# Kernel tuning notes

Hardware: AMD Instinct MI355X
Metric: run time of the kernel (lower is better)

The kernel has to match this reference:

```python
import jax, jax.numpy as jnp
import numpy as np

B, C, T, H, W = 8, 1024, 8, 28, 28
E = C // 2  # embed_dim = 512
EPS = 1e-5


def conv1x1(x, w, b):
    # x: [B,C,T,H,W], w: [O,C], b: [O] -> [B,O,T,H,W]
    return jnp.einsum('bcthw,oc->bothw', x, w) + b[None, :, None, None, None]


def maxpool_122(x):
    # MaxPool3d(kernel=(1,2,2)), stride = kernel, VALID padding
    return jax.lax.reduce_window(
        x, -jnp.inf, jax.lax.max,
        window_dimensions=(1, 1, 1, 2, 2),
        window_strides=(1, 1, 1, 2, 2),
        padding='VALID')


def setup_inputs() -> dict:
    key = jax.random.key(0)
    ks = jax.random.split(key, 10)
    s_in = 1.0 / np.sqrt(C)
    s_e = 1.0 / np.sqrt(E)
    return {
        'x': jax.random.normal(ks[0], (B, C, T, H, W), dtype=jnp.float32),
        'w_theta': jax.random.normal(ks[1], (E, C), dtype=jnp.float32) * s_in,
        'b_theta': jnp.zeros((E,), dtype=jnp.float32),
        'w_phi': jax.random.normal(ks[2], (E, C), dtype=jnp.float32) * s_in,
        'b_phi': jnp.zeros((E,), dtype=jnp.float32),
        'w_g': jax.random.normal(ks[3], (E, C), dtype=jnp.float32) * s_in,
        'b_g': jnp.zeros((E,), dtype=jnp.float32),
        'w_out': jax.random.normal(ks[4], (C, E), dtype=jnp.float32) * s_e,
        'b_out': jnp.zeros((C,), dtype=jnp.float32),
        'bn_gamma': jnp.ones((C,), dtype=jnp.float32),
        'bn_beta': jnp.zeros((C,), dtype=jnp.float32),
        'bn_mean': jnp.zeros((C,), dtype=jnp.float32),
        'bn_var': jnp.ones((C,), dtype=jnp.float32),
    }


def reference(x, w_theta, b_theta, w_phi, b_phi, w_g, b_g,
              w_out, b_out, bn_gamma, bn_beta, bn_mean, bn_var):
    # embed projections (phi/g applied after (1,2,2) max-pool sub-sampling)
    theta = conv1x1(x, w_theta, b_theta).reshape(B, E, -1)      # [B,E,N]
    x_sub = maxpool_122(x)                                       # [B,C,T,H/2,W/2]
    phi = conv1x1(x_sub, w_phi, b_phi).reshape(B, E, -1)         # [B,E,M]
    g = conv1x1(x_sub, w_g, b_g).reshape(B, E, -1)               # [B,E,M]

    # gaussian non-local: softmax(theta^T phi) over keys
    scores = jnp.einsum('ben,bem->bnm', theta, phi)              # [B,N,M]
    p = jax.nn.softmax(scores, axis=2)

    y = jnp.einsum('bem,bnm->ben', g, p).reshape(B, E, T, H, W)  # [B,E,T,H,W]

    # W conv + BN (inference stats) + residual
    z = conv1x1(y, w_out, b_out)
    inv = jax.lax.rsqrt(bn_var + EPS)
    z = (z - bn_mean[None, :, None, None, None]) * (bn_gamma * inv)[None, :, None, None, None] \
        + bn_beta[None, :, None, None, None]
    return z + x
```

## Files before the change

kernel.cpp:

```cpp
#include <hip/hip_runtime.h>
#include <cstddef>

typedef _Float16 f16x8 __attribute__((ext_vector_type(8)));
typedef float f32x4 __attribute__((ext_vector_type(4)));

#define B_ 8
#define C_ 1024
#define T_ 8
#define H_ 28
#define W_ 28
#define E_ 512
#define N_ (T_*H_*W_)
#define M_ (T_*(H_/2)*(W_/2))

__device__ __forceinline__ void gld16(const _Float16* g, _Float16* l) {
    __builtin_amdgcn_global_load_lds((const __attribute__((address_space(1))) void*)g,
                                     (__attribute__((address_space(3))) void*)l, 16, 0, 0);
}

__global__ void prep_kernel(const float* __restrict__ wt, const float* __restrict__ wp,
                            const float* __restrict__ wg, const float* __restrict__ wo,
                            const float* __restrict__ b_out,
                            const float* __restrict__ gamma, const float* __restrict__ beta,
                            const float* __restrict__ mean, const float* __restrict__ var,
                            _Float16* __restrict__ wt_h, _Float16* __restrict__ wp_h,
                            _Float16* __restrict__ wg_h, _Float16* __restrict__ wo_h,
                            float* __restrict__ scale, float* __restrict__ shift,
                            int nW, int nC)
{
    int i = blockIdx.x * blockDim.x + threadIdx.x;
    if (i < nW) {
        wt_h[i] = (_Float16)wt[i];
        wp_h[i] = (_Float16)wp[i];
        wg_h[i] = (_Float16)wg[i];
        wo_h[i] = (_Float16)wo[i];
    }
    if (i < nC) {
        float sc = gamma[i] * rsqrtf(var[i] + 1e-5f);
        scale[i] = sc;
        shift[i] = (b_out[i] - mean[i]) * sc + beta[i];
    }
}

__global__ void xt_kernel(const float* __restrict__ x, _Float16* __restrict__ XT)
{
    __shared__ float sm[32][33];
    int n0 = blockIdx.x * 32, c0 = blockIdx.y * 32, b = blockIdx.z;
    const float* xb = x + (size_t)b * C_ * N_;
    _Float16* xtb = XT + (size_t)b * N_ * C_;
#pragma unroll
    for (int i = 0; i < 4; i++) {
        int c = c0 + threadIdx.y + i * 8;
        sm[threadIdx.y + i * 8][threadIdx.x] = xb[(size_t)c * N_ + n0 + threadIdx.x];
    }
    __syncthreads();
#pragma unroll
    for (int i = 0; i < 4; i++) {
        int n = n0 + threadIdx.y + i * 8;
        xtb[(size_t)n * C_ + c0 + threadIdx.x] = (_Float16)sm[threadIdx.x][threadIdx.y + i * 8];
    }
}

__global__ void pool_kernel(const float* __restrict__ x, _Float16* __restrict__ XST)
{
    __shared__ float sm[32][33];
    const int H2 = H_ / 2, W2 = W_ / 2, HW = H_ * W_;
    int m0 = blockIdx.x * 32, c0 = blockIdx.y * 32, b = blockIdx.z;
    const float* xb = x + (size_t)b * C_ * T_ * HW;
#pragma unroll
    for (int i = 0; i < 4; i++) {
        int c = c0 + threadIdx.y + i * 8;
        int m = m0 + threadIdx.x;
        int t = m / (H2 * W2);
        int r = m - t * (H2 * W2);
        int h2 = r / W2;
        int w2 = r - h2 * W2;
        const float* p = xb + ((size_t)c * T_ + t) * HW + (h2 * 2) * W_ + w2 * 2;
        float v0 = fmaxf(p[0], p[1]);
        float v1 = fmaxf(p[W_], p[W_ + 1]);
        sm[threadIdx.y + i * 8][threadIdx.x] = fmaxf(v0, v1);
    }
    __syncthreads();
#pragma unroll
    for (int i = 0; i < 4; i++) {
        int m = m0 + threadIdx.y + i * 8;
        XST[((size_t)b * M_ + m) * C_ + c0 + threadIdx.x] = (_Float16)sm[threadIdx.x][threadIdx.y + i * 8];
    }
}

__global__ void softmax_kernel(_Float16* __restrict__ S, int rows)
{
    int wave = threadIdx.x >> 6, lane = threadIdx.x & 63;
    int row = blockIdx.x * 4 + wave;
    if (row >= rows) return;
    _Float16* s = S + (size_t)row * M_;
    f16x8 v[4];
    bool val[4];
    float mx = -3.4e38f;
#pragma unroll
    for (int it = 0; it < 4; it++) {
        int base = it * 512 + lane * 8;
        val[it] = (base < M_);
        if (val[it]) {
            v[it] = *(const f16x8*)(s + base);
#pragma unroll
            for (int q = 0; q < 8; q++) mx = fmaxf(mx, (float)v[it][q]);
        }
    }
#pragma unroll
    for (int off = 32; off > 0; off >>= 1) mx = fmaxf(mx, __shfl_xor(mx, off, 64));
    float ev[32];
    float sum = 0.f;
#pragma unroll
    for (int it = 0; it < 4; it++) {
        if (val[it]) {
#pragma unroll
            for (int q = 0; q < 8; q++) {
                float e = __expf((float)v[it][q] - mx);
                ev[it * 8 + q] = e;
                sum += e;
            }
        }
    }
#pragma unroll
    for (int off = 32; off > 0; off >>= 1) sum += __shfl_xor(sum, off, 64);
    float inv = 1.f / sum;
#pragma unroll
    for (int it = 0; it < 4; it++) {
        if (val[it]) {
            f16x8 o;
#pragma unroll
            for (int q = 0; q < 8; q++) o[q] = (_Float16)(ev[it * 8 + q] * inv);
            *(f16x8*)(s + it * 512 + lane * 8) = o;
        }
    }
}

template<int BIAS, int EPI>
__global__ __launch_bounds__(256, 2)
void gemm_nt(const _Float16* __restrict__ A, const _Float16* __restrict__ B,
             void* __restrict__ Cout, const float* __restrict__ bias,
             const float* __restrict__ scale, const float* __restrict__ shift,
             const float* __restrict__ resid,
             int Mdim, int Ndim, int K,
             long long strideA, long long strideB, long long strideC)
{
    __shared__ alignas(16) _Float16 As[128 * 32];
    __shared__ alignas(16) _Float16 Bs[128 * 32];
    __shared__ alignas(16) float eps_[32 * 132];

    const int tid = threadIdx.x;
    const int lane = tid & 63;
    const int wave = tid >> 6;
    const int wm = wave >> 1, wn = wave & 1;
    const int lane15 = lane & 15, quad = lane >> 4;

    const int m0 = blockIdx.y * 128;
    const int n0 = blockIdx.x * 128;
    const int bz = blockIdx.z;
    A += (size_t)bz * strideA;
    B += (size_t)bz * strideB;

    const int c0 = wave * 128 + lane;
    const int c1 = c0 + 64;
    const int ar0 = min(m0 + (c0 >> 2), Mdim - 1);
    const int ar1 = min(m0 + (c1 >> 2), Mdim - 1);
    const int br0 = min(n0 + (c0 >> 2), Ndim - 1);
    const int br1 = min(n0 + (c1 >> 2), Ndim - 1);
    const _Float16* ap0 = A + (size_t)ar0 * K + (c0 & 3) * 8;
    const _Float16* ap1 = A + (size_t)ar1 * K + (c1 & 3) * 8;
    const _Float16* bp0 = B + (size_t)br0 * K + (c0 & 3) * 8;
    const _Float16* bp1 = B + (size_t)br1 * K + (c1 & 3) * 8;
    _Float16* lA0 = As + wave * 1024;
    _Float16* lA1 = As + wave * 1024 + 512;
    _Float16* lB0 = Bs + wave * 1024;
    _Float16* lB1 = Bs + wave * 1024 + 512;

    f32x4 acc[4][4];
#pragma unroll
    for (int i = 0; i < 4; i++)
#pragma unroll
        for (int j = 0; j < 4; j++)
            acc[i][j] = (f32x4){0.f, 0.f, 0.f, 0.f};

    for (int k0 = 0; k0 < K; k0 += 32) {
        __syncthreads();
        gld16(ap0 + k0, lA0);
        gld16(ap1 + k0, lA1);
        gld16(bp0 + k0, lB0);
        gld16(bp1 + k0, lB1);
        __syncthreads();

        f16x8 af[4], bf[4];
#pragma unroll
        for (int i = 0; i < 4; i++)
            af[i] = *(const f16x8*)&As[(wm * 64 + i * 16 + lane15) * 32 + quad * 8];
#pragma unroll
        for (int j = 0; j < 4; j++)
            bf[j] = *(const f16x8*)&Bs[(wn * 64 + j * 16 + lane15) * 32 + quad * 8];
#pragma unroll
        for (int i = 0; i < 4; i++)
#pragma unroll
            for (int j = 0; j < 4; j++)
                acc[i][j] = __builtin_amdgcn_mfma_f32_16x16x32_f16(af[i], bf[j], acc[i][j], 0, 0, 0);
    }

    const size_t cbase = (size_t)bz * strideC;
#pragma unroll
    for (int i = 0; i < 4; i++) {
        __syncthreads();
#pragma unroll
        for (int j = 0; j < 4; j++) {
            int col = wn * 64 + j * 16 + lane15;
#pragma unroll
            for (int r = 0; r < 4; r++)
                eps_[(wm * 16 + quad * 4 + r) * 132 + col] = acc[i][j][r];
        }
        __syncthreads();
        if (EPI == 2) {
            int rg = tid >> 5, cc = tid & 31;
#pragma unroll
            for (int r = 0; r < 4; r++) {
                int lr = rg * 4 + r;
                int grow = m0 + (lr >> 4) * 64 + i * 16 + (lr & 15);
                int gcol = n0 + cc * 4;
                size_t idx = cbase + (size_t)grow * Ndim + gcol;
                f32x4 v = *(const f32x4*)&eps_[lr * 132 + cc * 4];
                f32x4 res = *(const f32x4*)&resid[idx];
                float sc = scale[grow], sh = shift[grow];
                f32x4 o;
#pragma unroll
                for (int q = 0; q < 4; q++) o[q] = v[q] * sc + sh + res[q];
                *(f32x4*)&((float*)Cout)[idx] = o;
            }
        } else {
            int rg = tid >> 4, cc8 = tid & 15;
#pragma unroll
            for (int r2 = 0; r2 < 2; r2++) {
                int lr = rg * 2 + r2;
                int grow = m0 + (lr >> 4) * 64 + i * 16 + (lr & 15);
                int gcol = n0 + cc8 * 8;
                if (grow < Mdim && gcol < Ndim) {
                    f16x8 o;
#pragma unroll
                    for (int q = 0; q < 8; q++) {
                        float v2 = eps_[lr * 132 + cc8 * 8 + q];
                        if (BIAS == 1) v2 += bias[gcol + q];
                        if (BIAS == 2) v2 += bias[grow];
                        o[q] = (_Float16)v2;
                    }
                    *(f16x8*)&((_Float16*)Cout)[cbase + (size_t)grow * Ndim + gcol] = o;
                }
            }
        }
    }
}

extern "C" void kernel_launch(void* const* d_in, const int* in_sizes, int n_in,
                              void* d_out, int out_size, void* d_ws, size_t ws_size,
                              hipStream_t stream)
{
    const float* x       = (const float*)d_in[0];
    const float* w_theta = (const float*)d_in[1];
    const float* b_theta = (const float*)d_in[2];
    const float* w_phi   = (const float*)d_in[3];
    const float* b_phi   = (const float*)d_in[4];
    const float* w_g     = (const float*)d_in[5];
    const float* b_g     = (const float*)d_in[6];
    const float* w_out   = (const float*)d_in[7];
    const float* b_out   = (const float*)d_in[8];
    const float* gamma   = (const float*)d_in[9];
    const float* beta    = (const float*)d_in[10];
    const float* mean    = (const float*)d_in[11];
    const float* var     = (const float*)d_in[12];
    float* out = (float*)d_out;
    (void)in_sizes; (void)n_in; (void)out_size;

    char* ws = (char*)d_ws;
    size_t off = 0;
    auto alloc = [&](size_t bytes) -> void* {
        off = (off + 255) & ~(size_t)255;
        void* p = ws + off;
        off += bytes;
        return p;
    };

    _Float16* wt_h = (_Float16*)alloc((size_t)E_ * C_ * 2);
    _Float16* wp_h = (_Float16*)alloc((size_t)E_ * C_ * 2);
    _Float16* wg_h = (_Float16*)alloc((size_t)E_ * C_ * 2);
    _Float16* wo_h = (_Float16*)alloc((size_t)C_ * E_ * 2);
    float* scale   = (float*)alloc((size_t)C_ * 4);
    float* shift   = (float*)alloc((size_t)C_ * 4);
    _Float16* XT   = (_Float16*)alloc((size_t)B_ * N_ * C_ * 2);
    _Float16* XST  = (_Float16*)alloc((size_t)B_ * M_ * C_ * 2);
    _Float16* Th   = (_Float16*)alloc((size_t)B_ * N_ * E_ * 2);
    _Float16* Ph   = (_Float16*)alloc((size_t)B_ * M_ * E_ * 2);
    _Float16* Gb   = (_Float16*)alloc((size_t)B_ * E_ * M_ * 2);
    _Float16* Yt   = (_Float16*)alloc((size_t)B_ * N_ * E_ * 2);

    size_t sz_s_all = (size_t)B_ * N_ * M_ * 2;
    bool batched = ws_size > off + sz_s_all + 65536;
    _Float16* Sall = (_Float16*)alloc(batched ? sz_s_all : (size_t)N_ * M_ * 2);

    prep_kernel<<<dim3((E_ * C_) / 256), dim3(256), 0, stream>>>(
        w_theta, w_phi, w_g, w_out, b_out, gamma, beta, mean, var,
        wt_h, wp_h, wg_h, wo_h, scale, shift, E_ * C_, C_);

    xt_kernel<<<dim3(N_ / 32, C_ / 32, B_), dim3(32, 8), 0, stream>>>(x, XT);
    pool_kernel<<<dim3(M_ / 32, C_ / 32, B_), dim3(32, 8), 0, stream>>>(x, XST);

    gemm_nt<1, 0><<<dim3(E_ / 128, N_ / 128, B_), dim3(256), 0, stream>>>(
        XT, wt_h, Th, b_theta, nullptr, nullptr, nullptr,
        N_, E_, C_, (long long)N_ * C_, 0, (long long)N_ * E_);

    gemm_nt<1, 0><<<dim3(E_ / 128, (M_ + 127) / 128, B_), dim3(256), 0, stream>>>(
        XST, wp_h, Ph, b_phi, nullptr, nullptr, nullptr,
        M_, E_, C_, (long long)M_ * C_, 0, (long long)M_ * E_);

    gemm_nt<2, 0><<<dim3((M_ + 127) / 128, E_ / 128, B_), dim3(256), 0, stream>>>(
        wg_h, XST, Gb, b_g, nullptr, nullptr, nullptr,
        E_, M_, C_, 0, (long long)M_ * C_, (long long)E_ * M_);

    const int nbz = batched ? B_ : 1;
    for (int b0 = 0; b0 < B_; b0 += nbz) {
        gemm_nt<0, 0><<<dim3((M_ + 127) / 128, N_ / 128, nbz), dim3(256), 0, stream>>>(
            Th + (size_t)b0 * N_ * E_, Ph + (size_t)b0 * M_ * E_, Sall,
            nullptr, nullptr, nullptr, nullptr,
            N_, M_, E_, (long long)N_ * E_, (long long)M_ * E_, (long long)N_ * M_);

        softmax_kernel<<<dim3((nbz * N_) / 4), dim3(256), 0, stream>>>(Sall, nbz * N_);

        gemm_nt<0, 0><<<dim3(E_ / 128, N_ / 128, nbz), dim3(256), 0, stream>>>(
            Sall, Gb + (size_t)b0 * E_ * M_, Yt + (size_t)b0 * N_ * E_,
            nullptr, nullptr, nullptr, nullptr,
            N_, E_, M_, (long long)N_ * M_, (long long)E_ * M_, (long long)N_ * E_);
    }

    gemm_nt<0, 2><<<dim3(N_ / 128, C_ / 128, B_), dim3(256), 0, stream>>>(
        wo_h, Yt, out, nullptr, scale, shift, x,
        C_, N_, E_, 0, (long long)N_ * E_, (long long)C_ * N_);
}
```

Measured before the change: 998.5 us.

## Add 256x256 8-wave pipelined MFMA GEMM and pad key dimension to 1792

Adds a new gemm8 kernel that uses 256x256 tiles with 512 threads, double-buffered LDS filled by direct global-to-LDS loads, XOR-swizzled layout, and interleaved MFMA/load phases with priority hints. The key dimension M (1568) is padded to 1792 so tiles divide evenly. Pool and softmax zero-fill the padded region so the extra columns contribute nothing to the attention product. It is used for the theta/phi/g projections and both attention GEMMs, aiming to raise MFMA utilisation and data reuse. The cost is extra padded work, more scratch memory, and heavier register and LDS use per block.

```diff
diff --git a/kernel.cpp b/kernel.cpp
--- a/kernel.cpp
+++ b/kernel.cpp
@@ -12,6 +12,7 @@
 #define E_ 512
 #define N_ (T_*H_*W_)
 #define M_ (T_*(H_/2)*(W_/2))
+#define MP_ 1792
 
 __device__ __forceinline__ void gld16(const _Float16* g, _Float16* l) {
     __builtin_amdgcn_global_load_lds((const __attribute__((address_space(1))) void*)g,
@@ -71,20 +72,24 @@
     for (int i = 0; i < 4; i++) {
         int c = c0 + threadIdx.y + i * 8;
         int m = m0 + threadIdx.x;
-        int t = m / (H2 * W2);
-        int r = m - t * (H2 * W2);
-        int h2 = r / W2;
-        int w2 = r - h2 * W2;
-        const float* p = xb + ((size_t)c * T_ + t) * HW + (h2 * 2) * W_ + w2 * 2;
-        float v0 = fmaxf(p[0], p[1]);
-        float v1 = fmaxf(p[W_], p[W_ + 1]);
-        sm[threadIdx.y + i * 8][threadIdx.x] = fmaxf(v0, v1);
+        float v = 0.f;
+        if (m < M_) {
+            int t = m / (H2 * W2);
+            int r = m - t * (H2 * W2);
+            int h2 = r / W2;
+            int w2 = r - h2 * W2;
+            const float* p = xb + ((size_t)c * T_ + t) * HW + (h2 * 2) * W_ + w2 * 2;
+            float v0 = fmaxf(p[0], p[1]);
+            float v1 = fmaxf(p[W_], p[W_ + 1]);
+            v = fmaxf(v0, v1);
+        }
+        sm[threadIdx.y + i * 8][threadIdx.x] = v;
     }
     __syncthreads();
 #pragma unroll
     for (int i = 0; i < 4; i++) {
         int m = m0 + threadIdx.y + i * 8;
-        XST[((size_t)b * M_ + m) * C_ + c0 + threadIdx.x] = (_Float16)sm[threadIdx.x][threadIdx.y + i * 8];
+        XST[((size_t)b * MP_ + m) * C_ + c0 + threadIdx.x] = (_Float16)sm[threadIdx.x][threadIdx.y + i * 8];
     }
 }
 
@@ -93,7 +98,7 @@
     int wave = threadIdx.x >> 6, lane = threadIdx.x & 63;
     int row = blockIdx.x * 4 + wave;
     if (row >= rows) return;
-    _Float16* s = S + (size_t)row * M_;
+    _Float16* s = S + (size_t)row * MP_;
     f16x8 v[4];
     bool val[4];
     float mx = -3.4e38f;
@@ -127,11 +132,201 @@
     float inv = 1.f / sum;
 #pragma unroll
     for (int it = 0; it < 4; it++) {
+        int base = it * 512 + lane * 8;
         if (val[it]) {
             f16x8 o;
 #pragma unroll
             for (int q = 0; q < 8; q++) o[q] = (_Float16)(ev[it * 8 + q] * inv);
-            *(f16x8*)(s + it * 512 + lane * 8) = o;
+            *(f16x8*)(s + base) = o;
+        } else if (base < MP_) {
+            f16x8 z = {0, 0, 0, 0, 0, 0, 0, 0};
+            *(f16x8*)(s + base) = z;
+        }
+    }
+}
+
+template<int BIAS>
+__global__ __launch_bounds__(512, 2)
+void gemm8(const _Float16* __restrict__ A, const _Float16* __restrict__ B,
+           _Float16* __restrict__ Cout, const float* __restrict__ bias,
+           int Mdim, int Ndim, int K,
+           long long strideA, long long strideB, long long strideC)
+{
+    __shared__ alignas(16) _Float16 sA[2][256 * 64];
+    __shared__ alignas(16) _Float16 sB[2][256 * 64];
+
+    const int tid = threadIdx.x;
+    const int lane = tid & 63;
+    const int wave = tid >> 6;
+    const int wm = wave >> 2;
+    const int wn = wave & 3;
+    const int lane15 = lane & 15;
+    const int quad = lane >> 4;
+
+    const int n0 = blockIdx.x * 256;
+    const int m0 = blockIdx.y * 256;
+    A += (size_t)blockIdx.z * strideA;
+    B += (size_t)blockIdx.z * strideB;
+
+    const int ci = wave * 128 + lane;
+    const int row_q0 = ci >> 3;
+    const int klc = (ci & 7) ^ (row_q0 & 7);
+
+    const _Float16* ap[2][2];
+    const _Float16* bp[2][2];
+#pragma unroll
+    for (int q = 0; q < 2; q++)
+#pragma unroll
+        for (int h = 0; h < 2; h++) {
+            int rw = row_q0 + q * 8;
+            ap[q][h] = A + (size_t)min(m0 + h * 128 + rw, Mdim - 1) * K + klc * 8;
+            bp[q][h] = B + (size_t)min(n0 + h * 128 + rw, Ndim - 1) * K + klc * 8;
+        }
+
+    f32x4 acc[8][4];
+#pragma unroll
+    for (int i = 0; i < 8; i++)
+#pragma unroll
+        for (int j = 0; j < 4; j++) acc[i][j] = (f32x4){0.f, 0.f, 0.f, 0.f};
+
+    f16x8 af[4][2];
+    f16x8 bf[2][2][2];
+
+    char* sAc = (char*)sA;
+    char* sBc = (char*)sB;
+
+    auto stage_a = [&](int buf, int h, int kt) {
+        gld16(ap[0][h] + kt * 64, (_Float16*)(sAc + buf * 32768 + h * 16384 + wave * 2048));
+        gld16(ap[1][h] + kt * 64, (_Float16*)(sAc + buf * 32768 + h * 16384 + wave * 2048 + 1024));
+    };
+    auto stage_b = [&](int buf, int h, int kt) {
+        gld16(bp[0][h] + kt * 64, (_Float16*)(sBc + buf * 32768 + h * 16384 + wave * 2048));
+        gld16(bp[1][h] + kt * 64, (_Float16*)(sBc + buf * 32768 + h * 16384 + wave * 2048 + 1024));
+    };
+    auto rd_a = [&](int buf, int qr) {
+#pragma unroll
+        for (int rf = 0; rf < 4; rf++)
+#pragma unroll
+            for (int ks = 0; ks < 2; ks++) {
+                int row = wm * 128 + qr * 64 + rf * 16 + lane15;
+                int c = (ks * 4 + quad) ^ (row & 7);
+                af[rf][ks] = *(const f16x8*)(sAc + buf * 32768 + row * 128 + c * 16);
+            }
+    };
+    auto rd_b = [&](int buf, int qc) {
+#pragma unroll
+        for (int cf = 0; cf < 2; cf++)
+#pragma unroll
+            for (int ks = 0; ks < 2; ks++) {
+                int row = wn * 64 + qc * 32 + cf * 16 + lane15;
+                int c = (ks * 4 + quad) ^ (row & 7);
+                bf[qc][cf][ks] = *(const f16x8*)(sBc + buf * 32768 + row * 128 + c * 16);
+            }
+    };
+    auto mm = [&](int qr, int qc) {
+        __builtin_amdgcn_s_setprio(1);
+#pragma unroll
+        for (int rf = 0; rf < 4; rf++)
+#pragma unroll
+            for (int cf = 0; cf < 2; cf++)
+#pragma unroll
+                for (int ks = 0; ks < 2; ks++)
+                    acc[qr * 4 + rf][qc * 2 + cf] = __builtin_amdgcn_mfma_f32_16x16x32_f16(
+                        af[rf][ks], bf[qc][cf][ks], acc[qr * 4 + rf][qc * 2 + cf], 0, 0, 0);
+        __builtin_amdgcn_s_setprio(0);
+    };
+
+#define BAR() __builtin_amdgcn_s_barrier()
+#define WAIT_LGKM() do { asm volatile("s_waitcnt lgkmcnt(0)" ::: "memory"); \
+                         __builtin_amdgcn_sched_barrier(0); } while (0)
+#define WAIT_VM4() asm volatile("s_waitcnt vmcnt(4)" ::: "memory")
+
+    const int nIter = K >> 7;
+    const int ktMax = (K >> 6) - 1;
+
+    stage_a(0, 0, 0); stage_a(0, 1, 0);
+    stage_b(0, 0, 0); stage_b(0, 1, 0);
+    stage_b(1, 0, 1); stage_b(1, 1, 1);
+    WAIT_VM4();
+    BAR();
+
+    for (int t = 0; t < nIter; t++) {
+        const int k1 = 2 * t + 1;
+        const int k2 = min(2 * t + 2, ktMax);
+        const int k3 = min(2 * t + 3, ktMax);
+        rd_a(0, 0); rd_b(0, 0);
+        stage_a(1, 0, k1);
+        BAR(); WAIT_LGKM(); mm(0, 0); BAR();
+        rd_b(0, 1);
+        stage_a(1, 1, k1);
+        BAR(); WAIT_LGKM(); mm(0, 1); BAR();
+        rd_a(0, 1);
+        stage_b(0, 0, k2);
+        BAR(); WAIT_LGKM(); mm(1, 1); BAR();
+        stage_b(0, 1, k2);
+        BAR(); WAIT_LGKM(); mm(1, 0);
+        WAIT_VM4();
+        BAR();
+        rd_a(1, 0); rd_b(1, 0);
+        stage_a(0, 0, k2);
+        BAR(); WAIT_LGKM(); mm(0, 0); BAR();
+        rd_b(1, 1);
+        stage_a(0, 1, k2);
+        BAR(); WAIT_LGKM(); mm(0, 1); BAR();
+        rd_a(1, 1);
+        stage_b(1, 0, k3);
+        BAR(); WAIT_LGKM(); mm(1, 1); BAR();
+        stage_b(1, 1, k3);
+        BAR(); WAIT_LGKM(); mm(1, 0);
+        WAIT_VM4();
+        BAR();
+    }
+#undef BAR
+#undef WAIT_LGKM
+#undef WAIT_VM4
+
+    asm volatile("s_waitcnt vmcnt(0)" ::: "memory");
+    __syncthreads();
+    float* slab = (float*)sAc;
+    const size_t cbase = (size_t)blockIdx.z * strideC;
+#pragma unroll
+    for (int i = 0; i < 8; i++) {
+        __syncthreads();
+#pragma unroll
+        for (int cf = 0; cf < 4; cf++) {
+            int col = wn * 64 + (cf >> 1) * 32 + (cf & 1) * 16 + lane15;
+            int srb = wm * 16 + quad * 4;
+#pragma unroll
+            for (int r = 0; r < 4; r++)
+                slab[(srb + r) * 268 + col] = acc[i][cf][r];
+        }
+        __syncthreads();
+        int sr = tid & 31, cb = tid >> 5;
+        int g = m0 + (sr >> 4) * 128 + (i >> 2) * 64 + (i & 3) * 16 + (sr & 15);
+        if (g < Mdim) {
+            int gcol = n0 + cb * 16;
+            float vv[16];
+#pragma unroll
+            for (int k4 = 0; k4 < 4; k4++) {
+                f32x4 v = *(const f32x4*)&slab[sr * 268 + cb * 16 + k4 * 4];
+#pragma unroll
+                for (int j = 0; j < 4; j++) vv[k4 * 4 + j] = v[j];
+            }
+            if (BIAS == 1) {
+#pragma unroll
+                for (int j = 0; j < 16; j++) vv[j] += bias[gcol + j];
+            }
+            if (BIAS == 2) {
+                float bb = bias[g];
+#pragma unroll
+                for (int j = 0; j < 16; j++) vv[j] += bb;
+            }
+            f16x8 o0, o1;
+#pragma unroll
+            for (int j = 0; j < 8; j++) { o0[j] = (_Float16)vv[j]; o1[j] = (_Float16)vv[8 + j]; }
+            _Float16* cp = Cout + cbase + (size_t)g * Ndim + gcol;
+            *(f16x8*)cp = o0;
+            *(f16x8*)(cp + 8) = o1;
         }
     }
 }
@@ -292,48 +487,48 @@
     float* scale   = (float*)alloc((size_t)C_ * 4);
     float* shift   = (float*)alloc((size_t)C_ * 4);
     _Float16* XT   = (_Float16*)alloc((size_t)B_ * N_ * C_ * 2);
-    _Float16* XST  = (_Float16*)alloc((size_t)B_ * M_ * C_ * 2);
+    _Float16* XST  = (_Float16*)alloc((size_t)B_ * MP_ * C_ * 2);
     _Float16* Th   = (_Float16*)alloc((size_t)B_ * N_ * E_ * 2);
-    _Float16* Ph   = (_Float16*)alloc((size_t)B_ * M_ * E_ * 2);
-    _Float16* Gb   = (_Float16*)alloc((size_t)B_ * E_ * M_ * 2);
+    _Float16* Ph   = (_Float16*)alloc((size_t)B_ * MP_ * E_ * 2);
+    _Float16* Gb   = (_Float16*)alloc((size_t)B_ * E_ * MP_ * 2);
     _Float16* Yt   = (_Float16*)alloc((size_t)B_ * N_ * E_ * 2);
 
-    size_t sz_s_all = (size_t)B_ * N_ * M_ * 2;
+    size_t sz_s_all = (size_t)B_ * N_ * MP_ * 2;
     bool batched = ws_size > off + sz_s_all + 65536;
-    _Float16* Sall = (_Float16*)alloc(batched ? sz_s_all : (size_t)N_ * M_ * 2);
+    _Float16* Sall = (_Float16*)alloc(batched ? sz_s_all : (size_t)N_ * MP_ * 2);
 
     prep_kernel<<<dim3((E_ * C_) / 256), dim3(256), 0, stream>>>(
         w_theta, w_phi, w_g, w_out, b_out, gamma, beta, mean, var,
         wt_h, wp_h, wg_h, wo_h, scale, shift, E_ * C_, C_);
 
     xt_kernel<<<dim3(N_ / 32, C_ / 32, B_), dim3(32, 8), 0, stream>>>(x, XT);
-    pool_kernel<<<dim3(M_ / 32, C_ / 32, B_), dim3(32, 8), 0, stream>>>(x, XST);
-
-    gemm_nt<1, 0><<<dim3(E_ / 128, N_ / 128, B_), dim3(256), 0, stream>>>(
-        XT, wt_h, Th, b_theta, nullptr, nullptr, nullptr,
-        N_, E_, C_, (long long)N_ * C_, 0, (long long)N_ * E_);
-
-    gemm_nt<1, 0><<<dim3(E_ / 128, (M_ + 127) / 128, B_), dim3(256), 0, stream>>>(
-        XST, wp_h, Ph, b_phi, nullptr, nullptr, nullptr,
-        M_, E_, C_, (long long)M_ * C_, 0, (long long)M_ * E_);
-
-    gemm_nt<2, 0><<<dim3((M_ + 127) / 128, E_ / 128, B_), dim3(256), 0, stream>>>(
-        wg_h, XST, Gb, b_g, nullptr, nullptr, nullptr,
-        E_, M_, C_, 0, (long long)M_ * C_, (long long)E_ * M_);
+    pool_kernel<<<dim3(MP_ / 32, C_ / 32, B_), dim3(32, 8), 0, stream>>>(x, XST);
+
+    gemm8<1><<<dim3(E_ / 256, (N_ + 255) / 256, B_), dim3(512), 0, stream>>>(
+        XT, wt_h, Th, b_theta, N_, E_, C_,
+        (long long)N_ * C_, 0, (long long)N_ * E_);
+
+    gemm8<1><<<dim3(E_ / 256, MP_ / 256, B_), dim3(512), 0, stream>>>(
+        XST, wp_h, Ph, b_phi, MP_, E_, C_,
+        (long long)MP_ * C_, 0, (long long)MP_ * E_);
+
+    gemm8<2><<<dim3(MP_ / 256, E_ / 256, B_), dim3(512), 0, stream>>>(
+        wg_h, XST, Gb, b_g, E_, MP_, C_,
+        0, (long long)MP_ * C_, (long long)E_ * MP_);
 
     const int nbz = batched ? B_ : 1;
     for (int b0 = 0; b0 < B_; b0 += nbz) {
-        gemm_nt<0, 0><<<dim3((M_ + 127) / 128, N_ / 128, nbz), dim3(256), 0, stream>>>(
-            Th + (size_t)b0 * N_ * E_, Ph + (size_t)b0 * M_ * E_, Sall,
-            nullptr, nullptr, nullptr, nullptr,
-            N_, M_, E_, (long long)N_ * E_, (long long)M_ * E_, (long long)N_ * M_);
+        gemm8<0><<<dim3(MP_ / 256, (N_ + 255) / 256, nbz), dim3(512), 0, stream>>>(
+            Th + (size_t)b0 * N_ * E_, Ph + (size_t)b0 * MP_ * E_, Sall, nullptr,
+            N_, MP_, E_,
+            (long long)N_ * E_, (long long)MP_ * E_, (long long)N_ * MP_);
 
         softmax_kernel<<<dim3((nbz * N_) / 4), dim3(256), 0, stream>>>(Sall, nbz * N_);
 
-        gemm_nt<0, 0><<<dim3(E_ / 128, N_ / 128, nbz), dim3(256), 0, stream>>>(
-            Sall, Gb + (size_t)b0 * E_ * M_, Yt + (size_t)b0 * N_ * E_,
-            nullptr, nullptr, nullptr, nullptr,
-            N_, E_, M_, (long long)N_ * M_, (long long)E_ * M_, (long long)N_ * E_);
+        gemm8<0><<<dim3(E_ / 256, (N_ + 255) / 256, nbz), dim3(512), 0, stream>>>(
+            Sall, Gb + (size_t)b0 * E_ * MP_, Yt + (size_t)b0 * N_ * E_, nullptr,
+            N_, E_, MP_,
+            (long long)N_ * MP_, (long long)E_ * MP_, (long long)N_ * E_);
     }
 
     gemm_nt<0, 2><<<dim3(N_ / 128, C_ / 128, B_), dim3(256), 0, stream>>>(
```

After: 1.004 ms. Within noise of the previous version (+0.5%).
